# Kernel tuning notes

Hardware: AMD Instinct MI355X
Metric: run time of the kernel (lower is better)

Reference implementation:

```python
import jax, jax.numpy as jnp
import numpy as np

BUCKETS = 32
DIM = 1024
HEADS = 16
TEMP = 0.75
SINK_ITERS = 7
LOG_EPS = 1e-6
GUMBEL_EPS = 1e-4


def _sinkhorn(r, n_iters):
    # iterative row/col log-normalization, then exp (matches torch loop)
    for _ in range(n_iters):
        r = r - jax.scipy.special.logsumexp(r, axis=2, keepdims=True)
        r = r - jax.scipy.special.logsumexp(r, axis=1, keepdims=True)
    return jnp.exp(r)


def setup_inputs() -> dict:
    key = jax.random.key(0)
    kq, kk, kv, kw, kg = jax.random.split(key, 5)
    B, H, T, DH = 4, 16, 4096, 64
    q = jax.random.normal(kq, (B, H, T, DH), jnp.float32)
    k = jax.random.normal(kk, (B, H, T, DH), jnp.float32)
    v = jax.random.normal(kv, (B, H, T, DH), jnp.float32)
    sort_w = jax.random.normal(kw, (1, H, DH, BUCKETS), jnp.float32)
    u = jax.random.uniform(kg, (B * H, BUCKETS, BUCKETS), jnp.float32, 0.0, 1.0)
    gumbel_noise = -jnp.log(-jnp.log(u + GUMBEL_EPS) + GUMBEL_EPS)
    return {"q": q, "k": k, "v": v, "sort_w": sort_w, "gumbel_noise": gumbel_noise}


def reference(q, k, v, sort_w, gumbel_noise):
    b, h, t, dh = q.shape
    bh = b * h
    bsz = t // BUCKETS  # tokens per bucket
    # bucket: (bh, buckets, bsz, dh)
    qb = q.reshape(bh, BUCKETS, bsz, dh)
    kb = k.reshape(bh, BUCKETS, bsz, dh)
    vb = v.reshape(bh, BUCKETS, bsz, dh)
    # bucket summaries for routing
    b_k_r = kb.sum(axis=2)  # (bh, buckets, dh)
    e_w = jnp.broadcast_to(sort_w, (b, h, dh, BUCKETS)).reshape(bh, dh, BUCKETS)
    R = jnp.log(jax.nn.relu(jnp.einsum('bud,bdv->buv', b_k_r, e_w)) + LOG_EPS)
    R = (R + gumbel_noise) / TEMP
    R = _sinkhorn(R, SINK_ITERS)  # soft permutation matrix (bh, buckets, buckets)
    R = jnp.tril(R, -1)  # causal: only attend to strictly earlier buckets
    # soft-permute key/value buckets
    k_re = jnp.einsum('buv,bvtd->butd', R, kb)
    v_re = jnp.einsum('buv,bvtd->butd', R, vb)
    bk = jnp.concatenate([k_re, kb], axis=2)  # (bh, buckets, 2*bsz, dh)
    bv = jnp.concatenate([v_re, vb], axis=2)
    dots = jnp.einsum('buie,buje->buij', qb, bk) * (DIM ** -0.5)
    attn = jax.nn.softmax(dots, axis=-1)
    out = jnp.einsum('buij,buje->buie', attn, bv)  # (bh, buckets, bsz, dh)
    return out.reshape(b, h, t, dh)
```

## Files before the change

### kernel.cpp

```cpp
#include <hip/hip_runtime.h>
#include <hip/hip_bf16.h>

#define BUCKETS 32
#define BSZ 128
#define DH 64
#define TEMPINV 1.3333333333333333f
#define SINK_ITERS 7
#define LOG_EPS 1e-6f
#define SCALE 0.03125f

typedef short bf16x8 __attribute__((ext_vector_type(8)));
typedef float f32x4 __attribute__((ext_vector_type(4)));

__device__ __forceinline__ void bf8_to_f32(const uint4 x, float* f) {
    f[0] = __uint_as_float(x.x << 16);
    f[1] = __uint_as_float(x.x & 0xffff0000u);
    f[2] = __uint_as_float(x.y << 16);
    f[3] = __uint_as_float(x.y & 0xffff0000u);
    f[4] = __uint_as_float(x.z << 16);
    f[5] = __uint_as_float(x.z & 0xffff0000u);
    f[6] = __uint_as_float(x.w << 16);
    f[7] = __uint_as_float(x.w & 0xffff0000u);
}

__device__ __forceinline__ unsigned f2bf(float f) {
    unsigned x = __float_as_uint(f);
    return (x + 0x7fffu + ((x >> 16) & 1u)) >> 16;
}

__device__ __forceinline__ uint4 packbf8(const float* f) {
    uint4 r;
    r.x = f2bf(f[0]) | (f2bf(f[1]) << 16);
    r.y = f2bf(f[2]) | (f2bf(f[3]) << 16);
    r.z = f2bf(f[4]) | (f2bf(f[5]) << 16);
    r.w = f2bf(f[6]) | (f2bf(f[7]) << 16);
    return r;
}

__device__ __forceinline__ unsigned bfext(const uint4& w, int t) {
    const unsigned comp = (t < 2) ? w.x : (t < 4) ? w.y : (t < 6) ? w.z : w.w;
    return (t & 1) ? (comp >> 16) : (comp & 0xffffu);
}

__global__ __launch_bounds__(256) void route_kernel(
    const float* __restrict__ kptr,
    const float* __restrict__ swptr,
    const float* __restrict__ gptr,
    float* __restrict__ Rout)
{
    const int b = blockIdx.x;
    const int h = b & 15;
    const int tid = threadIdx.x;

    __shared__ float bkr[BUCKETS][DH];
    __shared__ float sw[DH][BUCKETS];
    __shared__ float R[BUCKETS][BUCKETS + 1];

    for (int o = tid; o < DH * BUCKETS; o += 256)
        sw[o >> 5][o & 31] = swptr[h * DH * BUCKETS + o];

    {
        const float4* k4 = (const float4*)kptr + (size_t)b * 65536;
        const int u = tid >> 3, g = tid & 7;
        float s[8] = {0.f,0.f,0.f,0.f,0.f,0.f,0.f,0.f};
        for (int i = 0; i < BSZ; ++i) {
            float4 a = k4[u * 2048 + i * 16 + g * 2];
            float4 c = k4[u * 2048 + i * 16 + g * 2 + 1];
            s[0] += a.x; s[1] += a.y; s[2] += a.z; s[3] += a.w;
            s[4] += c.x; s[5] += c.y; s[6] += c.z; s[7] += c.w;
        }
        for (int j = 0; j < 8; ++j) bkr[u][g * 8 + j] = s[j];
    }
    __syncthreads();

    for (int o = tid; o < BUCKETS * BUCKETS; o += 256) {
        const int uu = o >> 5, vv = o & 31;
        float dot = 0.f;
        for (int d = 0; d < DH; ++d) dot = fmaf(bkr[uu][d], sw[d][vv], dot);
        const float g = gptr[b * 1024 + o];
        R[uu][vv] = (logf(fmaxf(dot, 0.f) + LOG_EPS) + g) * TEMPINV;
    }
    __syncthreads();

    for (int it = 0; it < SINK_ITERS; ++it) {
        if (tid < BUCKETS) {
            float m = -1e30f;
            for (int j = 0; j < BUCKETS; ++j) m = fmaxf(m, R[tid][j]);
            float s = 0.f;
            for (int j = 0; j < BUCKETS; ++j) s += expf(R[tid][j] - m);
            const float lse = m + logf(s);
            for (int j = 0; j < BUCKETS; ++j) R[tid][j] -= lse;
        }
        __syncthreads();
        if (tid < BUCKETS) {
            float m = -1e30f;
            for (int j = 0; j < BUCKETS; ++j) m = fmaxf(m, R[j][tid]);
            float s = 0.f;
            for (int j = 0; j < BUCKETS; ++j) s += expf(R[j][tid] - m);
            const float lse = m + logf(s);
            for (int j = 0; j < BUCKETS; ++j) R[j][tid] -= lse;
        }
        __syncthreads();
    }

    for (int o = tid; o < BUCKETS * BUCKETS; o += 256) {
        const int uu = o >> 5, vv = o & 31;
        Rout[b * 1024 + o] = (vv < uu) ? expf(R[uu][vv]) : 0.f;
    }
}

__global__ __launch_bounds__(256) void reshuffle_kernel(
    const float* __restrict__ kptr,
    const float* __restrict__ vptr,
    const float* __restrict__ Rmat,
    uint4* __restrict__ kre,
    uint4* __restrict__ vre)
{
    const int cchunk = blockIdx.x;
    const int b = blockIdx.y;
    const int tid = threadIdx.x;

    __shared__ float lk[BUCKETS][64];
    __shared__ float lv[BUCKETS][64];
    __shared__ float lr[BUCKETS][BUCKETS + 1];

    const float4* kb4 = (const float4*)kptr + (size_t)b * 65536 + cchunk * 16;
    const float4* vb4 = (const float4*)vptr + (size_t)b * 65536 + cchunk * 16;

    for (int idx = tid; idx < 512; idx += 256) {
        const int v = idx >> 4, j = idx & 15;
        float4 t = kb4[v * 2048 + j];
        lk[v][j * 4 + 0] = t.x; lk[v][j * 4 + 1] = t.y;
        lk[v][j * 4 + 2] = t.z; lk[v][j * 4 + 3] = t.w;
        float4 s = vb4[v * 2048 + j];
        lv[v][j * 4 + 0] = s.x; lv[v][j * 4 + 1] = s.y;
        lv[v][j * 4 + 2] = s.z; lv[v][j * 4 + 3] = s.w;
    }
    for (int o = tid; o < 1024; o += 256)
        lr[o >> 5][o & 31] = Rmat[b * 1024 + o];
    __syncthreads();

    const int u = tid >> 3, c8 = tid & 7;
    float ka[8] = {0.f,0.f,0.f,0.f,0.f,0.f,0.f,0.f};
    float va[8] = {0.f,0.f,0.f,0.f,0.f,0.f,0.f,0.f};
    for (int vv = 0; vv < u; ++vv) {
        const float r = lr[u][vv];
        #pragma unroll
        for (int j = 0; j < 8; ++j) {
            ka[j] = fmaf(r, lk[vv][c8 * 8 + j], ka[j]);
            va[j] = fmaf(r, lv[vv][c8 * 8 + j], va[j]);
        }
    }
    const int oidx = b * 32768 + u * 1024 + cchunk * 8 + c8;
    kre[oidx] = packbf8(ka);
    vre[oidx] = packbf8(va);
}

__global__ __launch_bounds__(128) void attn_fallback(
    const float* __restrict__ qptr,
    const float* __restrict__ kptr,
    const float* __restrict__ vptr,
    const float* __restrict__ Rmat,
    float4* __restrict__ optr)
{
    const int u = blockIdx.x;
    const int b = blockIdx.y;
    const int tid = threadIdx.x;

    __shared__ uint4 sbk[2048];
    __shared__ uint4 sbv[2048];

    const float4* k4 = (const float4*)kptr + (size_t)b * 65536;
    const float4* v4 = (const float4*)vptr + (size_t)b * 65536;
    const float4* q4 = (const float4*)qptr + (size_t)b * 65536;

    const float* Rrow = Rmat + (b * BUCKETS + u) * BUCKETS;
    for (int o = tid; o < 1024; o += 128) {
        float ka[8] = {0.f,0.f,0.f,0.f,0.f,0.f,0.f,0.f};
        float va[8] = {0.f,0.f,0.f,0.f,0.f,0.f,0.f,0.f};
        for (int vv = 0; vv < u; ++vv) {
            const float r = Rrow[vv];
            float4 a = k4[vv * 2048 + 2 * o], c = k4[vv * 2048 + 2 * o + 1];
            ka[0] = fmaf(r, a.x, ka[0]); ka[1] = fmaf(r, a.y, ka[1]);
            ka[2] = fmaf(r, a.z, ka[2]); ka[3] = fmaf(r, a.w, ka[3]);
            ka[4] = fmaf(r, c.x, ka[4]); ka[5] = fmaf(r, c.y, ka[5]);
            ka[6] = fmaf(r, c.z, ka[6]); ka[7] = fmaf(r, c.w, ka[7]);
            float4 av = v4[vv * 2048 + 2 * o], cv = v4[vv * 2048 + 2 * o + 1];
            va[0] = fmaf(r, av.x, va[0]); va[1] = fmaf(r, av.y, va[1]);
            va[2] = fmaf(r, av.z, va[2]); va[3] = fmaf(r, av.w, va[3]);
            va[4] = fmaf(r, cv.x, va[4]); va[5] = fmaf(r, cv.y, va[5]);
            va[6] = fmaf(r, cv.z, va[6]); va[7] = fmaf(r, cv.w, va[7]);
        }
        sbk[o] = packbf8(ka);
        sbv[o] = packbf8(va);
        float4 a = k4[u * 2048 + 2 * o], c = k4[u * 2048 + 2 * o + 1];
        float f[8] = {a.x,a.y,a.z,a.w,c.x,c.y,c.z,c.w};
        sbk[1024 + o] = packbf8(f);
        float4 av = v4[u * 2048 + 2 * o], cv = v4[u * 2048 + 2 * o + 1];
        float g[8] = {av.x,av.y,av.z,av.w,cv.x,cv.y,cv.z,cv.w};
        sbv[1024 + o] = packbf8(g);
    }
    __syncthreads();

    const int i = tid;
    float qr[64];
    const float4* qrow = q4 + (u * 128 + i) * 16;
    for (int d4 = 0; d4 < 16; ++d4) {
        float4 t = qrow[d4];
        qr[d4 * 4 + 0] = t.x; qr[d4 * 4 + 1] = t.y;
        qr[d4 * 4 + 2] = t.z; qr[d4 * 4 + 3] = t.w;
    }

    float acc[64];
    for (int d = 0; d < 64; ++d) acc[d] = 0.f;
    float l = 0.f;

    for (int j = 0; j < 256; ++j) {
        float s = 0.f;
        for (int d8 = 0; d8 < 8; ++d8) {
            float f[8];
            bf8_to_f32(sbk[j * 8 + d8], f);
            for (int t = 0; t < 8; ++t) s = fmaf(qr[d8 * 8 + t], f[t], s);
        }
        const float p = __expf(s * SCALE);
        l += p;
        for (int d8 = 0; d8 < 8; ++d8) {
            float f[8];
            bf8_to_f32(sbv[j * 8 + d8], f);
            for (int t = 0; t < 8; ++t)
                acc[d8 * 8 + t] = fmaf(p, f[t], acc[d8 * 8 + t]);
        }
    }

    const float inv = 1.f / l;
    float4* orow = optr + (size_t)b * 65536 + (u * 128 + i) * 16;
    for (int d4 = 0; d4 < 16; ++d4) {
        float4 t;
        t.x = acc[d4 * 4 + 0] * inv;
        t.y = acc[d4 * 4 + 1] * inv;
        t.z = acc[d4 * 4 + 2] * inv;
        t.w = acc[d4 * 4 + 3] * inv;
        orow[d4] = t;
    }
}

__global__ __launch_bounds__(256) void attn_mfma(
    const float* __restrict__ qptr,
    const float* __restrict__ kptr,
    const float* __restrict__ vptr,
    const uint4* __restrict__ kre,
    const uint4* __restrict__ vre,
    float* __restrict__ optr)
{
    const int u = blockIdx.x;
    const int b = blockIdx.y;
    const int tid = threadIdx.x;
    const int lane = tid & 63;
    const int w = tid >> 6;
    const int lg = lane >> 4;
    const int lr = lane & 15;

    __shared__ uint4 sK[2048];
    __shared__ uint4 sV[2048];
    __shared__ uint4 sQ[1024];
    unsigned* sV32 = (unsigned*)sV;

    const float4* k4 = (const float4*)kptr + (size_t)b * 65536 + u * 2048;
    const float4* v4 = (const float4*)vptr + (size_t)b * 65536 + u * 2048;
    const float4* q4 = (const float4*)qptr + (size_t)b * 65536 + u * 2048;
    const uint4* kr = kre + (size_t)b * 32768 + u * 1024;
    const uint4* vr = vre + (size_t)b * 32768 + u * 1024;

    for (int m = tid; m < 1024; m += 256) {
        const int j = m >> 3, dc = m & 7;
        sK[j * 8 + (dc ^ (j & 7))] = kr[m];
    }
    for (int m = tid; m < 1024; m += 256) {
        const int j = m >> 3, dc = m & 7;
        const float4 a = k4[j * 16 + dc * 2];
        const float4 c = k4[j * 16 + dc * 2 + 1];
        float f[8] = {a.x, a.y, a.z, a.w, c.x, c.y, c.z, c.w};
        const int jj = 128 + j;
        sK[jj * 8 + (dc ^ (jj & 7))] = packbf8(f);
    }
    for (int qq = tid; qq < 512; qq += 256) {
        const int jp = qq >> 3, dc = qq & 7;
        const uint4 w0 = vr[jp * 16 + dc];
        const uint4 w1 = vr[jp * 16 + 8 + dc];
        unsigned* dst = sV32 + (jp >> 2) * 256 + (jp & 3);
        #pragma unroll
        for (int t = 0; t < 8; ++t) {
            const int blk = dc * 8 + (t ^ dc);
            dst[blk * 4] = bfext(w0, t) | (bfext(w1, t) << 16);
        }
    }
    for (int qq = tid; qq < 512; qq += 256) {
        const int jp = qq >> 3, dc = qq & 7;
        const float4 a0 = v4[(2 * jp) * 16 + dc * 2];
        const float4 c0 = v4[(2 * jp) * 16 + dc * 2 + 1];
        const float4 a1 = v4[(2 * jp + 1) * 16 + dc * 2];
        const float4 c1 = v4[(2 * jp + 1) * 16 + dc * 2 + 1];
        float f0[8] = {a0.x, a0.y, a0.z, a0.w, c0.x, c0.y, c0.z, c0.w};
        float f1[8] = {a1.x, a1.y, a1.z, a1.w, c1.x, c1.y, c1.z, c1.w};
        unsigned* dst = sV32 + (16 + (jp >> 2)) * 256 + (jp & 3);
        #pragma unroll
        for (int t = 0; t < 8; ++t) {
            const int blk = dc * 8 + (t ^ dc);
            dst[blk * 4] = f2bf(f0[t]) | (f2bf(f1[t]) << 16);
        }
    }
    for (int m = tid; m < 1024; m += 256) {
        const int j = m >> 3, dc = m & 7;
        const float4 a = q4[j * 16 + dc * 2];
        const float4 c = q4[j * 16 + dc * 2 + 1];
        float f[8] = {a.x * SCALE, a.y * SCALE, a.z * SCALE, a.w * SCALE,
                      c.x * SCALE, c.y * SCALE, c.z * SCALE, c.w * SCALE};
        sQ[j * 8 + (dc ^ (j & 7))] = packbf8(f);
    }
    __syncthreads();

    bf16x8 qf[2][2];
    #pragma unroll
    for (int mt = 0; mt < 2; ++mt)
        #pragma unroll
        for (int c = 0; c < 2; ++c) {
            const int row = w * 32 + mt * 16 + lr;
            const int dcu = c * 4 + lg;
            uint4 t = sQ[row * 8 + (dcu ^ (row & 7))];
            qf[mt][c] = *(bf16x8*)&t;
        }
    __syncthreads();

    uint4* sP = sQ + w * 256;
    unsigned short* sPh = (unsigned short*)sP;

    f32x4 acc[2][4];
    float lsum[2][4];
    #pragma unroll
    for (int mt = 0; mt < 2; ++mt) {
        #pragma unroll
        for (int nt = 0; nt < 4; ++nt) {
            acc[mt][nt][0] = 0.f; acc[mt][nt][1] = 0.f;
            acc[mt][nt][2] = 0.f; acc[mt][nt][3] = 0.f;
        }
        #pragma unroll
        for (int r = 0; r < 4; ++r) lsum[mt][r] = 0.f;
    }

    for (int kb = 0; kb < 4; ++kb) {
        bf16x8 kf[4][2];
        #pragma unroll
        for (int nt = 0; nt < 4; ++nt)
            #pragma unroll
            for (int c = 0; c < 2; ++c) {
                const int j = kb * 64 + nt * 16 + lr;
                const int dcu = c * 4 + lg;
                uint4 t = sK[j * 8 + (dcu ^ (j & 7))];
                kf[nt][c] = *(bf16x8*)&t;
            }
        f32x4 s[2][4];
        #pragma unroll
        for (int mt = 0; mt < 2; ++mt)
            #pragma unroll
            for (int nt = 0; nt < 4; ++nt) {
                s[mt][nt][0] = 0.f; s[mt][nt][1] = 0.f;
                s[mt][nt][2] = 0.f; s[mt][nt][3] = 0.f;
            }
        #pragma unroll
        for (int c = 0; c < 2; ++c)
            #pragma unroll
            for (int mt = 0; mt < 2; ++mt)
                #pragma unroll
                for (int nt = 0; nt < 4; ++nt)
                    s[mt][nt] = __builtin_amdgcn_mfma_f32_16x16x32_bf16(
                        qf[mt][c], kf[nt][c], s[mt][nt], 0, 0, 0);

        #pragma unroll
        for (int mt = 0; mt < 2; ++mt)
            #pragma unroll
            for (int nt = 0; nt < 4; ++nt)
                #pragma unroll
                for (int r = 0; r < 4; ++r) {
                    const float p = __expf(s[mt][nt][r]);
                    lsum[mt][r] += p;
                    const int row = mt * 16 + lg * 4 + r;
                    const int col = nt * 16 + lr;
                    sPh[row * 64 + (((col >> 3) ^ (row & 7)) << 3) + (col & 7)] =
                        (unsigned short)f2bf(p);
                }
        asm volatile("s_waitcnt lgkmcnt(0)" ::: "memory");
        __builtin_amdgcn_sched_barrier(0);

        bf16x8 pf[2][2];
        #pragma unroll
        for (int mt = 0; mt < 2; ++mt)
            #pragma unroll
            for (int c = 0; c < 2; ++c) {
                const int row = mt * 16 + lr;
                const int dcu = c * 4 + lg;
                uint4 t = sP[row * 8 + (dcu ^ (row & 7))];
                pf[mt][c] = *(bf16x8*)&t;
            }
        bf16x8 vf[4][2];
        #pragma unroll
        for (int nt = 0; nt < 4; ++nt)
            #pragma unroll
            for (int c = 0; c < 2; ++c) {
                const int p = kb * 8 + c * 4 + lg;
                const int d = nt * 16 + lr;
                const int blk = (d >> 3) * 8 + ((d & 7) ^ ((d >> 3) & 7));
                uint4 t = sV[p * 64 + blk];
                vf[nt][c] = *(bf16x8*)&t;
            }
        #pragma unroll
        for (int c = 0; c < 2; ++c)
            #pragma unroll
            for (int mt = 0; mt < 2; ++mt)
                #pragma unroll
                for (int nt = 0; nt < 4; ++nt)
                    acc[mt][nt] = __builtin_amdgcn_mfma_f32_16x16x32_bf16(
                        pf[mt][c], vf[nt][c], acc[mt][nt], 0, 0, 0);
    }

    #pragma unroll
    for (int mt = 0; mt < 2; ++mt)
        #pragma unroll
        for (int r = 0; r < 4; ++r) {
            float sum = lsum[mt][r];
            sum += __shfl_xor(sum, 1);
            sum += __shfl_xor(sum, 2);
            sum += __shfl_xor(sum, 4);
            sum += __shfl_xor(sum, 8);
            const float inv = 1.f / sum;
            const int row = mt * 16 + lg * 4 + r;
            float* orow = optr + (size_t)b * 262144 +
                          (size_t)(u * 128 + w * 32 + row) * 64;
            #pragma unroll
            for (int nt = 0; nt < 4; ++nt)
                orow[nt * 16 + lr] = acc[mt][nt][r] * inv;
        }
}

extern "C" void kernel_launch(void* const* d_in, const int* in_sizes, int n_in,
                              void* d_out, int out_size, void* d_ws, size_t ws_size,
                              hipStream_t stream) {
    const float* q  = (const float*)d_in[0];
    const float* k  = (const float*)d_in[1];
    const float* v  = (const float*)d_in[2];
    const float* sw = (const float*)d_in[3];
    const float* g  = (const float*)d_in[4];

    float* R   = (float*)d_ws;
    uint4* kre = (uint4*)((char*)d_ws + 262144);
    uint4* vre = (uint4*)((char*)d_ws + 262144 + 33554432);
    const bool big_ws = (ws_size >= (size_t)262144 + 2u * 33554432u);

    route_kernel<<<dim3(64), dim3(256), 0, stream>>>(k, sw, g, R);
    if (big_ws) {
        reshuffle_kernel<<<dim3(128, 64), dim3(256), 0, stream>>>(k, v, R, kre, vre);
        attn_mfma<<<dim3(32, 64), dim3(256), 0, stream>>>(q, k, v, kre, vre, (float*)d_out);
    } else {
        attn_fallback<<<dim3(32, 64), dim3(128), 0, stream>>>(q, k, v, R, (float4*)d_out);
    }
}
```

Measured before the change: 333.4 us.

## Split routing sum, prebuild swizzled bf16 K/V tile images, DMA into attention LDS

Bucket key sums move out of the 64-block routing kernel into a separate 2048-block reduction kernel, so the serial per-head sum no longer bottlenecks. The reshuffle kernel now writes complete pre-swizzled bf16 K and V tile images, both the permuted half and the original half, in the exact LDS layout the attention kernel expects. The attention kernel then fills LDS with direct global-to-LDS loads and converts Q straight from registers. Priority bumps are added around the MFMA sections. The trade-off is a doubled workspace, extra global traffic to write and reread the original K/V halves, and a higher workspace threshold, so the fallback path triggers on smaller workspaces.

```diff
diff --git a/kernel.cpp b/kernel.cpp
--- a/kernel.cpp
+++ b/kernel.cpp
@@ -37,13 +37,39 @@
     return r;
 }
 
-__device__ __forceinline__ unsigned bfext(const uint4& w, int t) {
-    const unsigned comp = (t < 2) ? w.x : (t < 4) ? w.y : (t < 6) ? w.z : w.w;
-    return (t & 1) ? (comp >> 16) : (comp & 0xffffu);
-}
-
-__global__ __launch_bounds__(256) void route_kernel(
-    const float* __restrict__ kptr,
+__device__ __forceinline__ void load_lds16(const uint4* g, uint4* l) {
+    __builtin_amdgcn_global_load_lds(
+        (const __attribute__((address_space(1))) unsigned int*)g,
+        (__attribute__((address_space(3))) unsigned int*)l, 16, 0, 0);
+}
+
+__global__ __launch_bounds__(256) void bksum_kernel(
+    const float* __restrict__ kptr, float* __restrict__ bkr)
+{
+    const int t = blockIdx.x;
+    const int tid = threadIdx.x;
+    __shared__ float4 part[16][17];
+    const float4* k4 = (const float4*)kptr + (size_t)t * 2048;
+    const int c4 = tid & 15, rg = tid >> 4;
+    float4 s; s.x = 0.f; s.y = 0.f; s.z = 0.f; s.w = 0.f;
+    for (int r = rg; r < 128; r += 16) {
+        float4 a = k4[r * 16 + c4];
+        s.x += a.x; s.y += a.y; s.z += a.z; s.w += a.w;
+    }
+    part[rg][c4] = s;
+    __syncthreads();
+    if (tid < 16) {
+        float4 acc = part[0][tid];
+        for (int g = 1; g < 16; ++g) {
+            float4 p = part[g][tid];
+            acc.x += p.x; acc.y += p.y; acc.z += p.z; acc.w += p.w;
+        }
+        ((float4*)bkr)[t * 16 + tid] = acc;
+    }
+}
+
+__global__ __launch_bounds__(256) void sinkhorn_kernel(
+    const float* __restrict__ bkrp,
     const float* __restrict__ swptr,
     const float* __restrict__ gptr,
     float* __restrict__ Rout)
@@ -52,31 +78,20 @@
     const int h = b & 15;
     const int tid = threadIdx.x;
 
-    __shared__ float bkr[BUCKETS][DH];
+    __shared__ float bk[BUCKETS][DH];
     __shared__ float sw[DH][BUCKETS];
     __shared__ float R[BUCKETS][BUCKETS + 1];
 
     for (int o = tid; o < DH * BUCKETS; o += 256)
         sw[o >> 5][o & 31] = swptr[h * DH * BUCKETS + o];
-
-    {
-        const float4* k4 = (const float4*)kptr + (size_t)b * 65536;
-        const int u = tid >> 3, g = tid & 7;
-        float s[8] = {0.f,0.f,0.f,0.f,0.f,0.f,0.f,0.f};
-        for (int i = 0; i < BSZ; ++i) {
-            float4 a = k4[u * 2048 + i * 16 + g * 2];
-            float4 c = k4[u * 2048 + i * 16 + g * 2 + 1];
-            s[0] += a.x; s[1] += a.y; s[2] += a.z; s[3] += a.w;
-            s[4] += c.x; s[5] += c.y; s[6] += c.z; s[7] += c.w;
-        }
-        for (int j = 0; j < 8; ++j) bkr[u][g * 8 + j] = s[j];
-    }
+    for (int o = tid; o < BUCKETS * DH; o += 256)
+        bk[o >> 6][o & 63] = bkrp[b * 2048 + o];
     __syncthreads();
 
     for (int o = tid; o < BUCKETS * BUCKETS; o += 256) {
         const int uu = o >> 5, vv = o & 31;
         float dot = 0.f;
-        for (int d = 0; d < DH; ++d) dot = fmaf(bkr[uu][d], sw[d][vv], dot);
+        for (int d = 0; d < DH; ++d) dot = fmaf(bk[uu][d], sw[d][vv], dot);
         const float g = gptr[b * 1024 + o];
         R[uu][vv] = (logf(fmaxf(dot, 0.f) + LOG_EPS) + g) * TEMPINV;
     }
@@ -109,51 +124,102 @@
     }
 }
 
-__global__ __launch_bounds__(256) void reshuffle_kernel(
+__global__ __launch_bounds__(256) void reshuffle2_kernel(
     const float* __restrict__ kptr,
     const float* __restrict__ vptr,
     const float* __restrict__ Rmat,
-    uint4* __restrict__ kre,
-    uint4* __restrict__ vre)
+    uint4* __restrict__ kimg,
+    uint4* __restrict__ vimg)
 {
-    const int cchunk = blockIdx.x;
-    const int b = blockIdx.y;
+    const int j0 = blockIdx.x;
+    const int b  = blockIdx.y;
     const int tid = threadIdx.x;
-
-    __shared__ float lk[BUCKETS][64];
-    __shared__ float lv[BUCKETS][64];
-    __shared__ float lr[BUCKETS][BUCKETS + 1];
-
-    const float4* kb4 = (const float4*)kptr + (size_t)b * 65536 + cchunk * 16;
-    const float4* vb4 = (const float4*)vptr + (size_t)b * 65536 + cchunk * 16;
-
-    for (int idx = tid; idx < 512; idx += 256) {
-        const int v = idx >> 4, j = idx & 15;
-        float4 t = kb4[v * 2048 + j];
-        lk[v][j * 4 + 0] = t.x; lk[v][j * 4 + 1] = t.y;
-        lk[v][j * 4 + 2] = t.z; lk[v][j * 4 + 3] = t.w;
-        float4 s = vb4[v * 2048 + j];
-        lv[v][j * 4 + 0] = s.x; lv[v][j * 4 + 1] = s.y;
-        lv[v][j * 4 + 2] = s.z; lv[v][j * 4 + 3] = s.w;
-    }
+    const int u = tid >> 3, c8 = tid & 7;
+
+    __shared__ float ls[32][8][64];
+    __shared__ float lr[32][33];
+
     for (int o = tid; o < 1024; o += 256)
         lr[o >> 5][o & 31] = Rmat[b * 1024 + o];
-    __syncthreads();
-
-    const int u = tid >> 3, c8 = tid & 7;
-    float ka[8] = {0.f,0.f,0.f,0.f,0.f,0.f,0.f,0.f};
-    float va[8] = {0.f,0.f,0.f,0.f,0.f,0.f,0.f,0.f};
-    for (int vv = 0; vv < u; ++vv) {
-        const float r = lr[u][vv];
-        #pragma unroll
-        for (int j = 0; j < 8; ++j) {
-            ka[j] = fmaf(r, lk[vv][c8 * 8 + j], ka[j]);
-            va[j] = fmaf(r, lv[vv][c8 * 8 + j], va[j]);
-        }
-    }
-    const int oidx = b * 32768 + u * 1024 + cchunk * 8 + c8;
-    kre[oidx] = packbf8(ka);
-    vre[oidx] = packbf8(va);
+
+    float4* ls4 = (float4*)ls;
+
+    {
+        const float4* kb4 = (const float4*)kptr + (size_t)b * 65536 + j0 * 128;
+        for (int it = 0; it < 16; ++it) {
+            const int idx = it * 256 + tid;
+            const int v = idx >> 7, i = idx & 127;
+            ls4[v * 128 + i] = kb4[v * 2048 + i];
+        }
+    }
+    __syncthreads();
+    {
+        float ka[8][8];
+        #pragma unroll
+        for (int r = 0; r < 8; ++r)
+            #pragma unroll
+            for (int t = 0; t < 8; ++t) ka[r][t] = 0.f;
+        for (int vv = 0; vv < u; ++vv) {
+            const float rw = lr[u][vv];
+            #pragma unroll
+            for (int r = 0; r < 8; ++r)
+                #pragma unroll
+                for (int t = 0; t < 8; ++t)
+                    ka[r][t] = fmaf(rw, ls[vv][r][c8 * 8 + t], ka[r][t]);
+        }
+        uint4* kdst = kimg + ((size_t)b * 32 + u) * 2048;
+        #pragma unroll
+        for (int r = 0; r < 8; ++r) {
+            kdst[(j0 * 8 + r) * 8 + (c8 ^ r)] = packbf8(ka[r]);
+            float o8[8];
+            #pragma unroll
+            for (int t = 0; t < 8; ++t) o8[t] = ls[u][r][c8 * 8 + t];
+            kdst[(128 + j0 * 8 + r) * 8 + (c8 ^ r)] = packbf8(o8);
+        }
+    }
+    __syncthreads();
+
+    {
+        const float4* vb4 = (const float4*)vptr + (size_t)b * 65536 + j0 * 128;
+        for (int it = 0; it < 16; ++it) {
+            const int idx = it * 256 + tid;
+            const int v = idx >> 7, i = idx & 127;
+            ls4[v * 128 + i] = vb4[v * 2048 + i];
+        }
+    }
+    __syncthreads();
+    {
+        float va[8][8];
+        #pragma unroll
+        for (int r = 0; r < 8; ++r)
+            #pragma unroll
+            for (int t = 0; t < 8; ++t) va[r][t] = 0.f;
+        for (int vv = 0; vv < u; ++vv) {
+            const float rw = lr[u][vv];
+            #pragma unroll
+            for (int r = 0; r < 8; ++r)
+                #pragma unroll
+                for (int t = 0; t < 8; ++t)
+                    va[r][t] = fmaf(rw, ls[vv][r][c8 * 8 + t], va[r][t]);
+        }
+        uint4* vdst = vimg + ((size_t)b * 32 + u) * 2048;
+        #pragma unroll
+        for (int t = 0; t < 8; ++t) {
+            const int blk = c8 * 8 + (t ^ c8);
+            uint4 wre;
+            wre.x = f2bf(va[0][t]) | (f2bf(va[1][t]) << 16);
+            wre.y = f2bf(va[2][t]) | (f2bf(va[3][t]) << 16);
+            wre.z = f2bf(va[4][t]) | (f2bf(va[5][t]) << 16);
+            wre.w = f2bf(va[6][t]) | (f2bf(va[7][t]) << 16);
+            vdst[j0 * 64 + blk] = wre;
+            uint4 wor;
+            wor.x = f2bf(ls[u][0][c8 * 8 + t]) | (f2bf(ls[u][1][c8 * 8 + t]) << 16);
+            wor.y = f2bf(ls[u][2][c8 * 8 + t]) | (f2bf(ls[u][3][c8 * 8 + t]) << 16);
+            wor.z = f2bf(ls[u][4][c8 * 8 + t]) | (f2bf(ls[u][5][c8 * 8 + t]) << 16);
+            wor.w = f2bf(ls[u][6][c8 * 8 + t]) | (f2bf(ls[u][7][c8 * 8 + t]) << 16);
+            vdst[(16 + j0) * 64 + blk] = wor;
+        }
+    }
 }
 
 __global__ __launch_bounds__(128) void attn_fallback(
@@ -244,12 +310,10 @@
     }
 }
 
-__global__ __launch_bounds__(256) void attn_mfma(
+__global__ __launch_bounds__(256) void attn_mfma2(
     const float* __restrict__ qptr,
-    const float* __restrict__ kptr,
-    const float* __restrict__ vptr,
-    const uint4* __restrict__ kre,
-    const uint4* __restrict__ vre,
+    const uint4* __restrict__ kimg,
+    const uint4* __restrict__ vimg,
     float* __restrict__ optr)
 {
     const int u = blockIdx.x;
@@ -262,77 +326,37 @@
 
     __shared__ uint4 sK[2048];
     __shared__ uint4 sV[2048];
-    __shared__ uint4 sQ[1024];
-    unsigned* sV32 = (unsigned*)sV;
-
-    const float4* k4 = (const float4*)kptr + (size_t)b * 65536 + u * 2048;
-    const float4* v4 = (const float4*)vptr + (size_t)b * 65536 + u * 2048;
-    const float4* q4 = (const float4*)qptr + (size_t)b * 65536 + u * 2048;
-    const uint4* kr = kre + (size_t)b * 32768 + u * 1024;
-    const uint4* vr = vre + (size_t)b * 32768 + u * 1024;
-
-    for (int m = tid; m < 1024; m += 256) {
-        const int j = m >> 3, dc = m & 7;
-        sK[j * 8 + (dc ^ (j & 7))] = kr[m];
-    }
-    for (int m = tid; m < 1024; m += 256) {
-        const int j = m >> 3, dc = m & 7;
-        const float4 a = k4[j * 16 + dc * 2];
-        const float4 c = k4[j * 16 + dc * 2 + 1];
-        float f[8] = {a.x, a.y, a.z, a.w, c.x, c.y, c.z, c.w};
-        const int jj = 128 + j;
-        sK[jj * 8 + (dc ^ (jj & 7))] = packbf8(f);
-    }
-    for (int qq = tid; qq < 512; qq += 256) {
-        const int jp = qq >> 3, dc = qq & 7;
-        const uint4 w0 = vr[jp * 16 + dc];
-        const uint4 w1 = vr[jp * 16 + 8 + dc];
-        unsigned* dst = sV32 + (jp >> 2) * 256 + (jp & 3);
-        #pragma unroll
-        for (int t = 0; t < 8; ++t) {
-            const int blk = dc * 8 + (t ^ dc);
-            dst[blk * 4] = bfext(w0, t) | (bfext(w1, t) << 16);
-        }
-    }
-    for (int qq = tid; qq < 512; qq += 256) {
-        const int jp = qq >> 3, dc = qq & 7;
-        const float4 a0 = v4[(2 * jp) * 16 + dc * 2];
-        const float4 c0 = v4[(2 * jp) * 16 + dc * 2 + 1];
-        const float4 a1 = v4[(2 * jp + 1) * 16 + dc * 2];
-        const float4 c1 = v4[(2 * jp + 1) * 16 + dc * 2 + 1];
-        float f0[8] = {a0.x, a0.y, a0.z, a0.w, c0.x, c0.y, c0.z, c0.w};
-        float f1[8] = {a1.x, a1.y, a1.z, a1.w, c1.x, c1.y, c1.z, c1.w};
-        unsigned* dst = sV32 + (16 + (jp >> 2)) * 256 + (jp & 3);
-        #pragma unroll
-        for (int t = 0; t < 8; ++t) {
-            const int blk = dc * 8 + (t ^ dc);
-            dst[blk * 4] = f2bf(f0[t]) | (f2bf(f1[t]) << 16);
-        }
-    }
-    for (int m = tid; m < 1024; m += 256) {
-        const int j = m >> 3, dc = m & 7;
-        const float4 a = q4[j * 16 + dc * 2];
-        const float4 c = q4[j * 16 + dc * 2 + 1];
-        float f[8] = {a.x * SCALE, a.y * SCALE, a.z * SCALE, a.w * SCALE,
-                      c.x * SCALE, c.y * SCALE, c.z * SCALE, c.w * SCALE};
-        sQ[j * 8 + (dc ^ (j & 7))] = packbf8(f);
-    }
-    __syncthreads();
-
+    __shared__ uint4 sP[1024];
+
+    const size_t tile = (size_t)b * 32 + u;
+    const uint4* gk = kimg + tile * 2048;
+    const uint4* gv = vimg + tile * 2048;
+
+    #pragma unroll
+    for (int it = 0; it < 8; ++it)
+        load_lds16(gk + it * 256 + tid, &sK[it * 256 + (w << 6)]);
+    #pragma unroll
+    for (int it = 0; it < 8; ++it)
+        load_lds16(gv + it * 256 + tid, &sV[it * 256 + (w << 6)]);
+
+    const float* qbase = qptr + (size_t)b * 262144 + (size_t)u * 8192;
     bf16x8 qf[2][2];
     #pragma unroll
     for (int mt = 0; mt < 2; ++mt)
         #pragma unroll
         for (int c = 0; c < 2; ++c) {
             const int row = w * 32 + mt * 16 + lr;
-            const int dcu = c * 4 + lg;
-            uint4 t = sQ[row * 8 + (dcu ^ (row & 7))];
-            qf[mt][c] = *(bf16x8*)&t;
-        }
-    __syncthreads();
-
-    uint4* sP = sQ + w * 256;
-    unsigned short* sPh = (unsigned short*)sP;
+            const float4* qr = (const float4*)(qbase + row * 64 + (c * 4 + lg) * 8);
+            float4 a = qr[0], cc = qr[1];
+            float f[8] = {a.x * SCALE, a.y * SCALE, a.z * SCALE, a.w * SCALE,
+                          cc.x * SCALE, cc.y * SCALE, cc.z * SCALE, cc.w * SCALE};
+            uint4 tq = packbf8(f);
+            qf[mt][c] = *(bf16x8*)&tq;
+        }
+    __syncthreads();
+
+    uint4* sPw = sP + w * 256;
+    unsigned short* sPh = (unsigned short*)sPw;
 
     f32x4 acc[2][4];
     float lsum[2][4];
@@ -366,6 +390,7 @@
                 s[mt][nt][0] = 0.f; s[mt][nt][1] = 0.f;
                 s[mt][nt][2] = 0.f; s[mt][nt][3] = 0.f;
             }
+        __builtin_amdgcn_s_setprio(1);
         #pragma unroll
         for (int c = 0; c < 2; ++c)
             #pragma unroll
@@ -374,6 +399,7 @@
                 for (int nt = 0; nt < 4; ++nt)
                     s[mt][nt] = __builtin_amdgcn_mfma_f32_16x16x32_bf16(
                         qf[mt][c], kf[nt][c], s[mt][nt], 0, 0, 0);
+        __builtin_amdgcn_s_setprio(0);
 
         #pragma unroll
         for (int mt = 0; mt < 2; ++mt)
@@ -398,7 +424,7 @@
             for (int c = 0; c < 2; ++c) {
                 const int row = mt * 16 + lr;
                 const int dcu = c * 4 + lg;
-                uint4 t = sP[row * 8 + (dcu ^ (row & 7))];
+                uint4 t = sPw[row * 8 + (dcu ^ (row & 7))];
                 pf[mt][c] = *(bf16x8*)&t;
             }
         bf16x8 vf[4][2];
@@ -412,6 +438,7 @@
                 uint4 t = sV[p * 64 + blk];
                 vf[nt][c] = *(bf16x8*)&t;
             }
+        __builtin_amdgcn_s_setprio(1);
         #pragma unroll
         for (int c = 0; c < 2; ++c)
             #pragma unroll
@@ -420,6 +447,7 @@
                 for (int nt = 0; nt < 4; ++nt)
                     acc[mt][nt] = __builtin_amdgcn_mfma_f32_16x16x32_bf16(
                         pf[mt][c], vf[nt][c], acc[mt][nt], 0, 0, 0);
+        __builtin_amdgcn_s_setprio(0);
     }
 
     #pragma unroll
@@ -450,15 +478,17 @@
     const float* sw = (const float*)d_in[3];
     const float* g  = (const float*)d_in[4];
 
-    float* R   = (float*)d_ws;
-    uint4* kre = (uint4*)((char*)d_ws + 262144);
-    uint4* vre = (uint4*)((char*)d_ws + 262144 + 33554432);
-    const bool big_ws = (ws_size >= (size_t)262144 + 2u * 33554432u);
-
-    route_kernel<<<dim3(64), dim3(256), 0, stream>>>(k, sw, g, R);
+    float* R    = (float*)d_ws;
+    float* bkr  = (float*)((char*)d_ws + 262144);
+    uint4* kimg = (uint4*)((char*)d_ws + 1048576);
+    uint4* vimg = (uint4*)((char*)d_ws + 1048576 + 67108864);
+    const bool big_ws = (ws_size >= (size_t)1048576 + 2u * 67108864u);
+
+    bksum_kernel<<<dim3(2048), dim3(256), 0, stream>>>(k, bkr);
+    sinkhorn_kernel<<<dim3(64), dim3(256), 0, stream>>>(bkr, sw, g, R);
     if (big_ws) {
-        reshuffle_kernel<<<dim3(128, 64), dim3(256), 0, stream>>>(k, v, R, kre, vre);
-        attn_mfma<<<dim3(32, 64), dim3(256), 0, stream>>>(q, k, v, kre, vre, (float*)d_out);
+        reshuffle2_kernel<<<dim3(16, 64), dim3(256), 0, stream>>>(k, v, R, kimg, vimg);
+        attn_mfma2<<<dim3(32, 64), dim3(256), 0, stream>>>(q, kimg, vimg, (float*)d_out);
     } else {
         attn_fallback<<<dim3(32, 64), dim3(128), 0, stream>>>(q, k, v, R, (float4*)d_out);
     }
```

Measured after the change: 328.8 us. No clear change (-1.4%).
